# Optimization experiments

Measured on AMD Instinct MI355X. Metric: run time of the kernel, lower is better.

The kernel has to match this reference:

```python
import jax, jax.numpy as jnp
import numpy as np

# dims
B, L, D = 16, 1024, 64          # batch, seq_len==node_num, d_model==feature_dim
DI, S, R, K = 128, 16, 4, 4     # d_inner=expand*d_model, d_state, dt_rank=ceil(D/16), conv kernel
H = 256                         # ffn hidden_dimention
N, ED, CK, PL = 1024, 10, 3, 96 # node_num, embed_dim, cheb_k, pred_len
NUM_LAYERS = 2


def setup_inputs() -> dict:
    key = jax.random.key(0)
    ks = iter(jax.random.split(key, 64))
    nrm = lambda shape, s=0.02: jax.random.normal(next(ks), shape, jnp.float32) * s
    inp = {"x": jax.random.normal(next(ks), (B, L, D), jnp.float32)}
    for pre in ("fw", "bw"):
        inp[pre + "_in"] = nrm((D, 2 * DI))
        inp[pre + "_conv_w"] = nrm((DI, K), 0.1)
        inp[pre + "_conv_b"] = jnp.zeros((DI,), jnp.float32)
        inp[pre + "_xproj"] = nrm((DI, R + 2 * S))
        inp[pre + "_dtw"] = nrm((R, DI))
        inp[pre + "_dtb"] = jnp.full((DI,), -4.6, jnp.float32)  # softplus -> small dt
        inp[pre + "_Alog"] = jnp.log(jnp.tile(jnp.arange(1, S + 1, dtype=jnp.float32), (DI, 1)))
        inp[pre + "_D"] = jnp.ones((DI,), jnp.float32)
        inp[pre + "_out"] = nrm((DI, D))
    inp["ln1_g"] = jnp.ones((D,), jnp.float32); inp["ln1_b"] = jnp.zeros((D,), jnp.float32)
    inp["ffn_w1"] = nrm((D, H)); inp["ffn_b1"] = jnp.zeros((H,), jnp.float32)
    inp["ffn_w2"] = nrm((H, D)); inp["ffn_b2"] = jnp.zeros((D,), jnp.float32)
    inp["ln2_g"] = jnp.ones((D,), jnp.float32); inp["ln2_b"] = jnp.zeros((D,), jnp.float32)
    inp["node_emb"] = nrm((N, ED), 0.1)
    inp["W_pool"] = nrm((ED, CK, D, D))
    inp["b_pool"] = nrm((ED, D))
    inp["proj_w"] = nrm((D, PL)); inp["proj_b"] = jnp.zeros((PL,), jnp.float32)
    return inp


def _layernorm(x, g, b):
    m = x.mean(-1, keepdims=True)
    v = ((x - m) ** 2).mean(-1, keepdims=True)
    return (x - m) * jax.lax.rsqrt(v + 1e-5) * g + b


def _mamba_dir(x, Wi, cw, cb, Wx, Wdt, bdt, Alog, Dp, Wo):
    # x: [B,L,D] -> selective-scan SSM output [B,L,D]
    Lx = x.shape[1]
    xz = x @ Wi                                   # [B,L,2*DI]
    xc, z = jnp.split(xz, 2, axis=-1)
    xp = jnp.pad(xc, ((0, 0), (K - 1, 0), (0, 0)))  # causal depthwise conv
    xc = sum(xp[:, k:k + Lx, :] * cw[:, k] for k in range(K)) + cb
    xc = jax.nn.silu(xc)
    dbc = xc @ Wx                                 # [B,L,R+2S]
    dt = jax.nn.softplus(dbc[..., :R] @ Wdt + bdt)  # [B,L,DI]
    Bm = dbc[..., R:R + S]                        # [B,L,S]
    Cm = dbc[..., R + S:]                         # [B,L,S]
    A = -jnp.exp(Alog)                            # [DI,S]
    dA = jnp.exp(dt[..., None] * A)               # [B,L,DI,S]
    dBx = dt[..., None] * Bm[:, :, None, :] * xc[..., None]  # [B,L,DI,S]

    def step(h, ins):
        dA_t, dBx_t, C_t = ins
        h = h * dA_t + dBx_t                      # [B,DI,S]
        y = jnp.einsum('bds,bs->bd', h, C_t)
        return h, y

    h0 = jnp.zeros((x.shape[0], DI, S), x.dtype)
    _, ys = jax.lax.scan(step, h0, (jnp.moveaxis(dA, 1, 0), jnp.moveaxis(dBx, 1, 0), jnp.moveaxis(Cm, 1, 0)))
    y = jnp.moveaxis(ys, 0, 1) + Dp * xc
    y = y * jax.nn.silu(z)
    return y @ Wo


def _forward(x,
             fw_in, fw_conv_w, fw_conv_b, fw_xproj, fw_dtw, fw_dtb, fw_Alog, fw_D, fw_out,
             bw_in, bw_conv_w, bw_conv_b, bw_xproj, bw_dtw, bw_dtb, bw_Alog, bw_D, bw_out,
             ln1_g, ln1_b, ffn_w1, ffn_b1, ffn_w2, ffn_b2, ln2_g, ln2_b,
             node_emb, W_pool, b_pool, proj_w, proj_b):
    # num_layers applications of the SAME (weight-tied) bidirectional Mamba block
    for _ in range(NUM_LAYERS):
        yf = _mamba_dir(x, fw_in, fw_conv_w, fw_conv_b, fw_xproj, fw_dtw, fw_dtb, fw_Alog, fw_D, fw_out)
        yb = jnp.flip(_mamba_dir(jnp.flip(x, 1), bw_in, bw_conv_w, bw_conv_b, bw_xproj, bw_dtw, bw_dtb, bw_Alog, bw_D, bw_out), 1)
        x = _layernorm(x + yf + yb, ln1_g, ln1_b)
        x = _layernorm(x + jax.nn.relu(x @ ffn_w1 + ffn_b1) @ ffn_w2 + ffn_b2, ln2_g, ln2_b)
    # adaptive Chebyshev graph convolution (AGCRN AVWGCN)
    sup = jax.nn.softmax(jax.nn.relu(node_emb @ node_emb.T), axis=-1)   # [N,N]
    cheb = [jnp.eye(N, dtype=x.dtype), sup]
    for _ in range(CK - 2):
        cheb.append(2.0 * (sup @ cheb[-1]) - cheb[-2])
    supports = jnp.stack(cheb)                                          # [CK,N,N]
    xg = jnp.einsum('knm,bmc->bknc', supports, x)                       # [B,CK,N,C]
    W = jnp.einsum('ne,ekio->nkio', node_emb, W_pool)                   # [N,CK,C,C]
    bias = node_emb @ b_pool                                            # [N,C]
    out = jnp.einsum('bknc,nkco->bno', xg, W) + bias                    # [B,N,C]
    # dropout is identity in eval; final projection to pred_len
    return out @ proj_w + proj_b                                        # [B,N,PL]


def reference(x,
              fw_in, fw_conv_w, fw_conv_b, fw_xproj, fw_dtw, fw_dtb, fw_Alog, fw_D, fw_out,
              bw_in, bw_conv_w, bw_conv_b, bw_xproj, bw_dtw, bw_dtb, bw_Alog, bw_D, bw_out,
              ln1_g, ln1_b, ffn_w1, ffn_b1, ffn_w2, ffn_b2, ln2_g, ln2_b,
              node_emb, W_pool, b_pool, proj_w, proj_b):
    return _forward(x,
                    fw_in, fw_conv_w, fw_conv_b, fw_xproj, fw_dtw, fw_dtb, fw_Alog, fw_D, fw_out,
                    bw_in, bw_conv_w, bw_conv_b, bw_xproj, bw_dtw, bw_dtb, bw_Alog, bw_D, bw_out,
                    ln1_g, ln1_b, ffn_w1, ffn_b1, ffn_w2, ffn_b2, ln2_g, ln2_b,
                    node_emb, W_pool, b_pool, proj_w, proj_b)
```

## Files before the change

### kernel.cpp

```cpp
#include <hip/hip_runtime.h>
#include <cstddef>

#define LSEQ   1024
#define BATCH  16
#define NSTATE 16
#define BLROWS 16384
#define NNODES 1024

typedef unsigned short ushort_t;
typedef __attribute__((ext_vector_type(8))) short short8;
typedef __attribute__((ext_vector_type(4))) float f32x4;

__device__ __forceinline__ ushort_t f2bf(float f){
  union { float f; unsigned u; } v; v.f = f;
  unsigned r = v.u + 0x7fffu + ((v.u >> 16) & 1u);
  return (ushort_t)(r >> 16);
}
__device__ __forceinline__ float bf2f(ushort_t u){
  union { unsigned u; float f; } v; v.u = ((unsigned)u) << 16; return v.f;
}
__device__ __forceinline__ unsigned cvtpk(float a, float b){
  unsigned r;
  asm("v_cvt_pk_bf16_f32 %0, %1, %2" : "=v"(r) : "v"(a), "v"(b));
  return r;
}

__global__ __launch_bounds__(256) void prep_kernel(
    const float* __restrict__ x, float* __restrict__ xc, ushort_t* __restrict__ xbf,
    const float* w0, const float* w1, const float* w2, const float* w3,
    const float* w4, const float* w5, const float* w6,
    const float* w7, const float* w8, ushort_t* dst)
{
  const int bi = blockIdx.x, tid = threadIdx.x;
  if (bi < 4096){
    int i = bi * 256 + tid;
    float v = x[i];
    xc[i] = v; xbf[i] = f2bf(v);
    return;
  }
  int blk = bi - 4096;
  if (blk == 0 || blk == 1){
    const float* src = blk ? w1 : w0;
    int off = blk ? 16384 : 0;
    for (int i = tid; i < 16384; i += 256){
      int n = i / 64, k = i % 64;
      dst[off + i] = f2bf(src[k * 256 + n]);
    }
  } else if (blk == 2 || blk == 3){
    const float* src = (blk == 3) ? w3 : w2;
    int coff = (blk == 3) ? 128 : 0;
    for (int i = tid; i < 8192; i += 256){
      int o = i / 128, k = i % 128;
      dst[32768 + o * 256 + coff + k] = f2bf(src[k * 64 + o]);
    }
  } else if (blk == 4){
    for (int i = tid; i < 16384; i += 256){
      int n = i / 64, k = i % 64;
      dst[49152 + i] = f2bf(w4[k * 256 + n]);
    }
  } else if (blk == 5){
    for (int i = tid; i < 16384; i += 256){
      int n = i / 256, k = i % 256;
      dst[65536 + i] = f2bf(w5[k * 64 + n]);
    }
  } else if (blk == 6){
    for (int i = tid; i < 6144; i += 256){
      int n = i / 64, k = i % 64;
      dst[81920 + i] = f2bf(w6[k * 96 + n]);
    }
  } else {
    const float* src = (blk == 8) ? w8 : w7;
    int off = (blk == 8) ? 96256 : 88064;
    for (int i = tid; i < 8192; i += 256){
      int n = i / 128, k = i % 128;
      dst[off + i] = (n < 36) ? f2bf(src[k * 36 + n]) : (ushort_t)0;
    }
  }
}

__global__ __launch_bounds__(256, 4) void scanblock_kernel(
    const ushort_t* __restrict__ dtRbf, const ushort_t* __restrict__ xcRbf,
    const float* __restrict__ BCm, const ushort_t* __restrict__ ZBF,
    const float* __restrict__ Df, const float* __restrict__ Db,
    const float* __restrict__ HIN,
    const ushort_t* __restrict__ WoT, const ushort_t* __restrict__ W1T,
    const ushort_t* __restrict__ W2T,
    const float* __restrict__ b1, const float* __restrict__ b2,
    const float* __restrict__ ln1g, const float* __restrict__ ln1b,
    const float* __restrict__ ln2g, const float* __restrict__ ln2b,
    float* __restrict__ XCUR, ushort_t* __restrict__ XCURbf)
{
  __shared__ float    BCl[1024];
  __shared__ ushort_t Ys[16 * 264];
  __shared__ float    x1f[16 * 68];
  __shared__ ushort_t x1b[16 * 72];
  __shared__ ushort_t Hs[16 * 264];
  __shared__ float    x2f[16 * 68];
  const int tid = threadIdx.x;
  const int lane = tid & 63, w = tid >> 6;
  const int l15 = lane & 15, quad = lane >> 4;
  const int row0 = blockIdx.x * 16;
  const int b = blockIdx.x >> 6, c = blockIdx.x & 63;
  const int n = w * 16 + l15;

  ((float4*)BCl)[tid] = ((const float4*)&BCm[(size_t)row0 * 64])[tid];
  __syncthreads();

  {
    const int half = tid >> 7, d = tid & 127;
    float h[NSTATE];
    {
      size_t base = ((((size_t)half * 16 + b) * 64 + c) * 16) * 128 + d;
#pragma unroll
      for (int s = 0; s < NSTATE; s++) h[s] = HIN[base + (size_t)s * 128];
    }
    const float Dv = half ? Db[d] : Df[d];

    for (int tt = 0; tt < 16; tt++){
      int t = half ? (15 - tt) : tt;
      int row = row0 + t;
      float dtv = bf2f(dtRbf[(size_t)row * 256 + half * 128 + d]);
      float xcv = bf2f(xcRbf[(size_t)row * 256 + half * 128 + d]);
      float sgz = bf2f(ZBF[(size_t)row * 256 + half * 128 + d]);
      float c0 = dtv * xcv;
      const float4* B4 = (const float4*)&BCl[t * 64 + half * 32];
      float4 b0 = B4[0], b1v = B4[1], b2v = B4[2], b3 = B4[3];
      float Bsr[NSTATE] = {b0.x,b0.y,b0.z,b0.w, b1v.x,b1v.y,b1v.z,b1v.w,
                           b2v.x,b2v.y,b2v.z,b2v.w, b3.x,b3.y,b3.z,b3.w};
      float4 c00 = B4[4], c1 = B4[5], c2 = B4[6], c3 = B4[7];
      float Csr[NSTATE] = {c00.x,c00.y,c00.z,c00.w, c1.x,c1.y,c1.z,c1.w,
                           c2.x,c2.y,c2.z,c2.w, c3.x,c3.y,c3.z,c3.w};
      float rv = __expf(-dtv);
      float r2 = rv * rv, r4p = r2 * r2;
      float dA0 = rv, dA1 = r2, dA2 = r2 * rv, dA3 = r4p;
      float ys0 = 0.f, ys1 = 0.f, ys2 = 0.f, ys3 = 0.f;
#pragma unroll
      for (int k = 0; k < 4; k++){
        int s = k * 4;
        h[s+0] = h[s+0] * dA0 + c0 * Bsr[s+0]; ys0 += h[s+0] * Csr[s+0];
        h[s+1] = h[s+1] * dA1 + c0 * Bsr[s+1]; ys1 += h[s+1] * Csr[s+1];
        h[s+2] = h[s+2] * dA2 + c0 * Bsr[s+2]; ys2 += h[s+2] * Csr[s+2];
        h[s+3] = h[s+3] * dA3 + c0 * Bsr[s+3]; ys3 += h[s+3] * Csr[s+3];
        if (k < 3){ dA0 *= r4p; dA1 *= r4p; dA2 *= r4p; dA3 *= r4p; }
      }
      float ys = (ys0 + ys1) + (ys2 + ys3);
      Ys[t * 264 + half * 128 + d] = f2bf((ys + Dv * xcv) * sgz);
    }
  }
  __syncthreads();

  {
    f32x4 acc = (f32x4){0.f, 0.f, 0.f, 0.f};
#pragma unroll
    for (int ks = 0; ks < 8; ks++){
      short8 a = *(const short8*)&Ys[l15 * 264 + ks * 32 + quad * 8];
      short8 bb = *(const short8*)&WoT[(size_t)n * 256 + ks * 32 + quad * 8];
      acc = __builtin_amdgcn_mfma_f32_16x16x32_bf16(a, bb, acc, 0, 0, 0);
    }
#pragma unroll
    for (int r = 0; r < 4; r++){
      int lr = quad * 4 + r;
      x1f[lr * 68 + n] = acc[r] + XCUR[(size_t)(row0 + lr) * 64 + n];
    }
  }
  __syncthreads();

  {
    int r = tid >> 4, li = tid & 15;
    float4 v = *(float4*)&x1f[r * 68 + li * 4];
    float s = v.x + v.y + v.z + v.w;
    s += __shfl_xor(s, 1); s += __shfl_xor(s, 2);
    s += __shfl_xor(s, 4); s += __shfl_xor(s, 8);
    float m = s * (1.f / 64.f);
    float q = (v.x-m)*(v.x-m) + (v.y-m)*(v.y-m) + (v.z-m)*(v.z-m) + (v.w-m)*(v.w-m);
    q += __shfl_xor(q, 1); q += __shfl_xor(q, 2);
    q += __shfl_xor(q, 4); q += __shfl_xor(q, 8);
    float wsc = rsqrtf(q * (1.f / 64.f) + 1e-5f);
    float vv[4] = {v.x, v.y, v.z, v.w};
#pragma unroll
    for (int j = 0; j < 4; j++){
      int col = li * 4 + j;
      float o = (vv[j] - m) * wsc * ln1g[col] + ln1b[col];
      x1f[r * 68 + col] = o;
      x1b[r * 72 + col] = f2bf(o);
    }
  }
  __syncthreads();

  {
    f32x4 acc1[4];
#pragma unroll
    for (int f = 0; f < 4; f++) acc1[f] = (f32x4){0.f, 0.f, 0.f, 0.f};
#pragma unroll
    for (int ks = 0; ks < 2; ks++){
      short8 a = *(const short8*)&x1b[l15 * 72 + ks * 32 + quad * 8];
#pragma unroll
      for (int f = 0; f < 4; f++){
        int hc = w * 64 + f * 16 + l15;
        short8 bb = *(const short8*)&W1T[(size_t)hc * 64 + ks * 32 + quad * 8];
        acc1[f] = __builtin_amdgcn_mfma_f32_16x16x32_bf16(a, bb, acc1[f], 0, 0, 0);
      }
    }
#pragma unroll
    for (int f = 0; f < 4; f++){
      int hc = w * 64 + f * 16 + l15;
      float bv = b1[hc];
#pragma unroll
      for (int r = 0; r < 4; r++)
        Hs[(quad * 4 + r) * 264 + hc] = f2bf(fmaxf(acc1[f][r] + bv, 0.f));
    }
  }
  __syncthreads();

  {
    f32x4 acc2 = (f32x4){0.f, 0.f, 0.f, 0.f};
#pragma unroll
    for (int ks = 0; ks < 8; ks++){
      short8 a = *(const short8*)&Hs[l15 * 264 + ks * 32 + quad * 8];
      short8 bb = *(const short8*)&W2T[(size_t)n * 256 + ks * 32 + quad * 8];
      acc2 = __builtin_amdgcn_mfma_f32_16x16x32_bf16(a, bb, acc2, 0, 0, 0);
    }
    float bv = b2[n];
#pragma unroll
    for (int r = 0; r < 4; r++){
      int lr = quad * 4 + r;
      x2f[lr * 68 + n] = acc2[r] + bv + x1f[lr * 68 + n];
    }
  }
  __syncthreads();

  {
    int r = tid >> 4, li = tid & 15;
    float4 v = *(float4*)&x2f[r * 68 + li * 4];
    float s = v.x + v.y + v.z + v.w;
    s += __shfl_xor(s, 1); s += __shfl_xor(s, 2);
    s += __shfl_xor(s, 4); s += __shfl_xor(s, 8);
    float m = s * (1.f / 64.f);
    float q = (v.x-m)*(v.x-m) + (v.y-m)*(v.y-m) + (v.z-m)*(v.z-m) + (v.w-m)*(v.w-m);
    q += __shfl_xor(q, 1); q += __shfl_xor(q, 2);
    q += __shfl_xor(q, 4); q += __shfl_xor(q, 8);
    float wsc = rsqrtf(q * (1.f / 64.f) + 1e-5f);
    float vv[4] = {v.x, v.y, v.z, v.w};
#pragma unroll
    for (int j = 0; j < 4; j++){
      int col = li * 4 + j;
      float o = (vv[j] - m) * wsc * ln2g[col] + ln2b[col];
      XCUR[(size_t)(row0 + r) * 64 + col] = o;
      XCURbf[(size_t)(row0 + r) * 64 + col] = f2bf(o);
    }
  }
}

__global__ __launch_bounds__(256) void dbcdt_kernel(
    const ushort_t* __restrict__ XB,
    const ushort_t* __restrict__ WIN,
    ushort_t* __restrict__ ZBF,
    const float* cwf, const float* cbf, const ushort_t* wxtf,
    const float* wdtf, const float* bdtf,
    const float* cwb, const float* cbb, const ushort_t* wxtb,
    const float* wdtb, const float* bdtb,
    ushort_t* __restrict__ xcRbf, ushort_t* __restrict__ dtRbf,
    float* __restrict__ BCm, float* __restrict__ HLOC, float* __restrict__ PST)
{
  __shared__ ushort_t As[32 * 72];
  __shared__ ushort_t xzl[19 * 132];
  __shared__ ushort_t dtl[16 * 136];
  __shared__ float dbcs[16][40];
  const int tid = threadIdx.x;
  const int lane = tid & 63, w = tid >> 6;
  const int l15 = lane & 15, quad = lane >> 4;
  const int dir = (blockIdx.x >= 1024) ? 1 : 0;
  const int chunk = blockIdx.x & 1023;
  const int row0 = chunk * 16;
  const int t0 = row0 & (LSEQ - 1);
  const float*    cw  = dir ? cwb  : cwf;
  const float*    cb  = dir ? cbb  : cbf;
  const ushort_t* WxT = dir ? wxtb : wxtf;
  const float*    Wdt = dir ? wdtb : wdtf;
  const float*    bdt = dir ? bdtb : bdtf;

  {
    const int abase = row0 + (dir ? 0 : -3);
    int r = tid >> 3, ko = (tid & 7) * 8;
    uint4 v = {0u, 0u, 0u, 0u};
    bool zero = (r >= 19) ||
                (dir == 0 && t0 == 0 && r < 3) ||
                (dir == 1 && t0 == LSEQ - 16 && r >= 16);
    if (!zero) v = *(const uint4*)&XB[(size_t)(abase + r) * 64 + ko];
    *(uint4*)&As[r * 72 + ko] = v;
  }
  __syncthreads();

  {
    f32x4 xacc[2][4];
#pragma unroll
    for (int mt = 0; mt < 2; mt++)
#pragma unroll
      for (int f = 0; f < 4; f++) xacc[mt][f] = (f32x4){0.f, 0.f, 0.f, 0.f};
    const ushort_t* Wd = &WIN[(size_t)dir * 256 * 64];
#pragma unroll
    for (int ks = 0; ks < 2; ks++){
      short8 a0 = *(const short8*)&As[(l15) * 72 + ks * 32 + quad * 8];
      short8 a1 = *(const short8*)&As[(16 + l15) * 72 + ks * 32 + quad * 8];
#pragma unroll
      for (int f = 0; f < 4; f++){
        short8 b = *(const short8*)&Wd[(size_t)((w * 4 + f) * 16 + l15) * 64 + ks * 32 + quad * 8];
        xacc[0][f] = __builtin_amdgcn_mfma_f32_16x16x32_bf16(a0, b, xacc[0][f], 0, 0, 0);
        xacc[1][f] = __builtin_amdgcn_mfma_f32_16x16x32_bf16(a1, b, xacc[1][f], 0, 0, 0);
      }
    }
    const int zoff = dir ? 0 : 3;
#pragma unroll
    for (int mt = 0; mt < 2; mt++){
#pragma unroll
      for (int f = 0; f < 4; f++){
        int col = (w * 4 + f) * 16 + l15;
        if (col < 128){
#pragma unroll
          for (int rp = 0; rp < 2; rp++){
            unsigned pk = cvtpk(xacc[mt][f][rp*2], xacc[mt][f][rp*2+1]);
            int rowl = mt * 16 + quad * 4 + rp * 2;
            if (rowl < 19)     xzl[rowl * 132 + col]       = (ushort_t)pk;
            if (rowl + 1 < 19) xzl[(rowl + 1) * 132 + col] = (ushort_t)(pk >> 16);
          }
        } else {
          int cz = col - 128;
#pragma unroll
          for (int rp = 0; rp < 2; rp++){
            float va = xacc[mt][f][rp*2], vb = xacc[mt][f][rp*2+1];
            va = va / (1.f + __expf(-va));
            vb = vb / (1.f + __expf(-vb));
            unsigned pk = cvtpk(va, vb);
            int rowl = mt * 16 + quad * 4 + rp * 2;
            int ta = rowl - zoff, tb = rowl + 1 - zoff;
            if ((unsigned)ta < 16u)
              ZBF[(size_t)(row0 + ta) * 256 + dir * 128 + cz] = (ushort_t)pk;
            if ((unsigned)tb < 16u)
              ZBF[(size_t)(row0 + tb) * 256 + dir * 128 + cz] = (ushort_t)(pk >> 16);
          }
        }
      }
    }
  }
  __syncthreads();

  const int dd0 = tid & 127;
  const int rb = tid >> 7;
  float cr[8];
  {
    float rowv[11];
#pragma unroll
    for (int j = 0; j < 11; j++)
      rowv[j] = bf2f(xzl[(rb * 8 + j) * 132 + dd0]);
    float w0 = cw[dd0*4+0], w1 = cw[dd0*4+1], w2 = cw[dd0*4+2], w3 = cw[dd0*4+3];
    float cbv = cb[dd0];
#pragma unroll
    for (int p = 0; p < 8; p++){
      float v;
      if (dir == 0)
        v = cbv + w0*rowv[p] + w1*rowv[p+1] + w2*rowv[p+2] + w3*rowv[p+3];
      else
        v = cbv + w3*rowv[p] + w2*rowv[p+1] + w1*rowv[p+2] + w0*rowv[p+3];
      float sig = 1.f / (1.f + __expf(-v));
      cr[p] = v * sig;
    }
  }
  __syncthreads();
  ushort_t* xcl = xzl;
#pragma unroll
  for (int p = 0; p < 4; p++){
    unsigned pk = cvtpk(cr[2*p], cr[2*p+1]);
    int r = rb * 8 + 2 * p;
    xcl[r * 136 + dd0]       = (ushort_t)pk;
    xcl[(r + 1) * 136 + dd0] = (ushort_t)(pk >> 16);
    xcRbf[(size_t)(row0 + r) * 256 + dir * 128 + dd0]     = (ushort_t)pk;
    xcRbf[(size_t)(row0 + r + 1) * 256 + dir * 128 + dd0] = (ushort_t)(pk >> 16);
  }
  __syncthreads();

  {
    f32x4 pacc = (f32x4){0.f,0.f,0.f,0.f};
#pragma unroll
    for (int ks = 0; ks < 4; ks++){
      short8 a = *(const short8*)&xcl[l15 * 136 + ks * 32 + quad * 8];
      short8 b = *(const short8*)&WxT[(size_t)(w * 16 + l15) * 128 + ks * 32 + quad * 8];
      pacc = __builtin_amdgcn_mfma_f32_16x16x32_bf16(a, b, pacc, 0, 0, 0);
    }
    int col = w * 16 + l15;
    if (col < 36){
#pragma unroll
      for (int r = 0; r < 4; r++)
        dbcs[quad * 4 + r][col] = pacc[r];
    }
  }
  __syncthreads();

  {
    float w0d = Wdt[dd0], w1d = Wdt[128 + dd0], w2d = Wdt[256 + dd0],
          w3d = Wdt[384 + dd0], b0d = bdt[dd0];
    float dtvv[8];
#pragma unroll
    for (int k = 0; k < 8; k++){
      int r = rb + 2 * k;
      float u = b0d + dbcs[r][0]*w0d + dbcs[r][1]*w1d
                    + dbcs[r][2]*w2d + dbcs[r][3]*w3d;
      dtvv[k] = (u > 20.f) ? u : __logf(1.f + __expf(u));
    }
#pragma unroll
    for (int k = 0; k < 4; k++){
      unsigned pk = cvtpk(dtvv[2*k], dtvv[2*k+1]);
      int r0 = rb + 4 * k, r1 = r0 + 2;
      dtl[r0 * 136 + dd0] = (ushort_t)pk;
      dtl[r1 * 136 + dd0] = (ushort_t)(pk >> 16);
      dtRbf[(size_t)(row0 + r0) * 256 + dir * 128 + dd0] = (ushort_t)pk;
      dtRbf[(size_t)(row0 + r1) * 256 + dir * 128 + dd0] = (ushort_t)(pk >> 16);
    }
  }
  {
    int r = tid >> 4, s = tid & 15;
    BCm[(size_t)(row0 + r) * 64 + dir * 32 + s]      = dbcs[r][4 + s];
    BCm[(size_t)(row0 + r) * 64 + dir * 32 + 16 + s] = dbcs[r][20 + s];
  }
  __syncthreads();

  {
    const int shalf = tid >> 7, d = tid & 127;
    const int b = chunk >> 6, c = chunk & 63;
    float h[8];
#pragma unroll
    for (int i = 0; i < 8; i++) h[i] = 0.f;
    float sdt = 0.f;
    for (int rr2 = 0; rr2 < 16; rr2++){
      int r = dir ? (15 - rr2) : rr2;
      float dtv = bf2f(dtl[r * 136 + d]);
      sdt += dtv;
      float rv = __expf(-dtv);
      float xcv = bf2f(xcl[r * 136 + d]);
      float c0 = dtv * xcv;
      float r2 = rv * rv, r4p = r2 * r2;
      float a0;
      if (shalf){ float r8 = r4p * r4p; a0 = r8 * rv; }
      else a0 = rv;
      float a1 = a0 * rv, a2 = a0 * r2, a3 = a1 * r2;
      const float* Bp = &dbcs[r][4 + shalf * 8];
      h[0] = h[0] * a0 + c0 * Bp[0];
      h[1] = h[1] * a1 + c0 * Bp[1];
      h[2] = h[2] * a2 + c0 * Bp[2];
      h[3] = h[3] * a3 + c0 * Bp[3];
      a0 *= r4p; a1 *= r4p; a2 *= r4p; a3 *= r4p;
      h[4] = h[4] * a0 + c0 * Bp[4];
      h[5] = h[5] * a1 + c0 * Bp[5];
      h[6] = h[6] * a2 + c0 * Bp[6];
      h[7] = h[7] * a3 + c0 * Bp[7];
    }
    float e1 = __expf(-sdt);
    float base;
    if (shalf){ float e2 = e1*e1, e4 = e2*e2, e8 = e4*e4; base = e8 * e1; }
    else base = e1;
    float P[8];
    P[0] = base;
#pragma unroll
    for (int i = 1; i < 8; i++) P[i] = P[i-1] * e1;

    size_t ob = ((((size_t)dir * 16 + b) * 64 + c) * 16 + shalf * 8) * 128 + d;
#pragma unroll
    for (int i = 0; i < 8; i++){
      HLOC[ob + (size_t)i * 128] = h[i];
      PST [ob + (size_t)i * 128] = P[i];
    }
  }
}

__global__ __launch_bounds__(512) void scan_p2_kernel(
    const float* __restrict__ HLOC, float* __restrict__ PST)
{
  __shared__ float hspec[4][128];
  __shared__ float qend[4][128];
  const int tid = threadIdx.x;
  const int d = tid & 127, seg = tid >> 7;
  const int bi = blockIdx.x;
  const int s = bi & 15, b = (bi >> 4) & 15, dir = bi >> 8;
  size_t base = (((size_t)(dir * 16 + b) * 64) * 16 + s) * 128 + d;

  float spec[16], Qa[16];
  float h = 0.f, Q = 1.f;
#pragma unroll
  for (int i = 0; i < 16; i++){
    int sp = seg * 16 + i;
    int c = dir ? (63 - sp) : sp;
    size_t o = base + (size_t)c * 2048;
    float hl = HLOC[o];
    float pv = PST[o];
    spec[i] = h; Qa[i] = Q;
    h = pv * h + hl;
    Q *= pv;
  }
  hspec[seg][d] = h;
  qend[seg][d] = Q;
  __syncthreads();
  float hin = 0.f;
  for (int j = 0; j < seg; j++) hin = hspec[j][d] + qend[j][d] * hin;
#pragma unroll
  for (int i = 0; i < 16; i++){
    int sp = seg * 16 + i;
    int c = dir ? (63 - sp) : sp;
    size_t o = base + (size_t)c * 2048;
    PST[o] = spec[i] + Qa[i] * hin;
  }
}

__global__ __launch_bounds__(256) void gprep_kernel(
    const float* __restrict__ E, ushort_t* __restrict__ supbf,
    const float* __restrict__ xcur, ushort_t* __restrict__ XTTbf,
    ushort_t* __restrict__ Acat,
    const float* __restrict__ Wp, ushort_t* __restrict__ WT2)
{
  __shared__ float smemf[5760];
  const int bi = blockIdx.x, tid = threadIdx.x;

  if (bi < 1024){
    float* wmax = smemf;
    float* wsum = smemf + 8;
    int n = bi;
    float e[10];
#pragma unroll
    for (int i = 0; i < 10; i++) e[i] = E[n * 10 + i];
    float vals[4]; float mx = 0.f;
#pragma unroll
    for (int j = 0; j < 4; j++){
      int m = tid + j * 256;
      const float* Em = &E[m * 10];
      float s = 0.f;
#pragma unroll
      for (int i = 0; i < 10; i++) s += e[i] * Em[i];
      s = fmaxf(s, 0.f);
      vals[j] = s; mx = fmaxf(mx, s);
    }
    for (int off = 32; off; off >>= 1) mx = fmaxf(mx, __shfl_xor(mx, off));
    if ((tid & 63) == 0) wmax[tid >> 6] = mx;
    __syncthreads();
    mx = fmaxf(fmaxf(wmax[0], wmax[1]), fmaxf(wmax[2], wmax[3]));
    float sum = 0.f;
#pragma unroll
    for (int j = 0; j < 4; j++){ vals[j] = __expf(vals[j] - mx); sum += vals[j]; }
    for (int off = 32; off; off >>= 1) sum += __shfl_xor(sum, off);
    if ((tid & 63) == 0) wsum[tid >> 6] = sum;
    __syncthreads();
    sum = wsum[0] + wsum[1] + wsum[2] + wsum[3];
    float inv = 1.f / sum;
#pragma unroll
    for (int j = 0; j < 4; j++)
      supbf[(size_t)n * NNODES + tid + j * 256] = f2bf(vals[j] * inv);
  } else if (bi < 1280){
    float (*tile)[65] = (float(*)[65])smemf;
    const int idx = bi - 1024;
    const int b = idx >> 4, nb = idx & 15;
    const int c = tid & 63, nr = tid >> 6;
#pragma unroll
    for (int p = 0; p < 16; p++){
      int n = nr + p * 4;
      float v = xcur[(((size_t)b << 10) + nb * 64 + n) * 64 + c];
      tile[n][c] = v;
    }
    __syncthreads();
#pragma unroll
    for (int p = 0; p < 16; p++){
      int n = nr + p * 4;
      Acat[(size_t)(nb * 64 + n) * 3072 + b * 192 + c] = f2bf(tile[n][c]);
    }
#pragma unroll
    for (int p = 0; p < 16; p++){
      int cc = nr + p * 4;
      int nn = c;
      XTTbf[(size_t)(b * 64 + cc) * 1024 + nb * 64 + nn] = f2bf(tile[nn][cc]);
    }
  } else {
    float* Es = smemf;
    float* Wt = smemf + 640;
    const int idx = bi - 1280;
    const int fk = idx % 24;
    const int fn = fk / 6, ks = fk % 6;
    const int g0 = (idx / 24) * 64;
    for (int i = tid; i < 640; i += 256) Es[i] = E[g0 * 10 + i];
    for (int i = tid; i < 5120; i += 256){
      int e = i >> 9, r = i & 511;
      int kcl = r >> 4, ol = r & 15;
      Wt[e * 512 + ol * 32 + kcl] =
          Wp[(size_t)e * 12288 + (ks * 32 + kcl) * 64 + fn * 16 + ol];
    }
    __syncthreads();
    const int nl = tid >> 2, kh = tid & 3;
    const float* Ev = &Es[nl * 10];
    ushort_t outv[128];
#pragma unroll
    for (int ol = 0; ol < 16; ol++){
#pragma unroll
      for (int jj = 0; jj < 8; jj++){
        int kc = kh * 8 + jj;
        float v = 0.f;
#pragma unroll
        for (int e = 0; e < 10; e++) v += Ev[e] * Wt[e * 512 + ol * 32 + kc];
        outv[ol * 8 + jj] = f2bf(v);
      }
    }
    size_t dst = (size_t)(g0 + nl) * 12288 + fk * 512 + kh * 128;
#pragma unroll
    for (int i = 0; i < 16; i++)
      *(uint4*)&WT2[dst + i * 8] = *(uint4*)&outv[i * 8];
  }
}

template<int MODE>
__global__ __launch_bounds__(256) void mfma_g_kernel(
    const ushort_t* __restrict__ Abf, const ushort_t* __restrict__ BTbf,
    ushort_t* __restrict__ CTbf, ushort_t* __restrict__ Acat)
{
  __shared__ ushort_t As[32 * 72];
  __shared__ ushort_t Bs[32 * 72];
  const int tid = threadIdx.x;
  const int lane = tid & 63, w = tid >> 6;
  const int bm = blockIdx.y, bn = blockIdx.x;
  const int mw = (w & 1) * 16, nw = (w >> 1) * 16;
  const int l15 = lane & 15, quad = lane >> 4;

  f32x4 acc = (f32x4){0.f, 0.f, 0.f, 0.f};

  const int ar = tid >> 3, ak = (tid & 7) * 8;
  const size_t agbase = (size_t)(bm * 32 + ar) * 1024 + ak;
  const size_t bgbase = (size_t)(bn * 32 + ar) * 1024 + ak;

  for (int k0 = 0; k0 < 1024; k0 += 64){
    *(uint4*)&As[ar * 72 + ak] = *(const uint4*)&Abf[agbase + k0];
    *(uint4*)&Bs[ar * 72 + ak] = *(const uint4*)&BTbf[bgbase + k0];
    __syncthreads();
#pragma unroll
    for (int ks = 0; ks < 2; ks++){
      short8 a = *(const short8*)&As[(mw + l15) * 72 + ks * 32 + quad * 8];
      short8 b = *(const short8*)&Bs[(nw + l15) * 72 + ks * 32 + quad * 8];
      acc = __builtin_amdgcn_mfma_f32_16x16x32_bf16(a, b, acc, 0, 0, 0);
    }
    __syncthreads();
  }

  {
    int gm0 = bm * 32 + mw + quad * 4;
    int gn  = bn * 32 + nw + l15;
    int bidx = gn >> 6, cidx = gn & 63;
    if (MODE == 0){
      unsigned long long pk = 0;
#pragma unroll
      for (int r = 0; r < 4; r++){
        ushort_t h = f2bf(acc[r]);
        pk |= (unsigned long long)h << (16 * r);
        Acat[(size_t)(gm0 + r) * 3072 + bidx * 192 + 64 + cidx] = h;
      }
      *(unsigned long long*)&CTbf[(size_t)gn * 1024 + gm0] = pk;
    } else {
#pragma unroll
      for (int r = 0; r < 4; r++){
        size_t arow = (size_t)(gm0 + r) * 3072 + bidx * 192;
        float xv = bf2f(Acat[arow + cidx]);
        Acat[arow + 128 + cidx] = f2bf(2.f * acc[r] - xv);
      }
    }
  }
}

__global__ __launch_bounds__(256) void out1_kernel(
    const ushort_t* __restrict__ Acat, const ushort_t* __restrict__ WT2,
    const ushort_t* __restrict__ pwT, const float* __restrict__ E,
    const float* __restrict__ bp, const float* __restrict__ pb,
    float* __restrict__ out)
{
  __shared__ ushort_t AsL[4 * 16 * 200];
  __shared__ ushort_t PW[96 * 72];
  __shared__ ushort_t o1s[4 * 16 * 72];
  __shared__ float biasn[4][64];
  const int tid = threadIdx.x;
  const int lane = tid & 63, w = tid >> 6;
  const int l15 = lane & 15, quad = lane >> 4;
  const int n0 = blockIdx.x * 4;

  for (int p = 0; p < 6; p++){
    int f8 = tid + p * 256;
    int idx = f8 * 8;
    int nl = idx / 3072, rem = idx % 3072;
    int b = rem / 192, kc = rem % 192;
    *(uint4*)&AsL[nl * 3200 + b * 200 + kc] =
        *(const uint4*)&Acat[(size_t)(n0 + nl) * 3072 + rem];
  }
  for (int p = 0; p < 3; p++){
    int f8 = tid + p * 256;
    int idx = f8 * 8;
    int pr = idx / 64, kk = idx % 64;
    *(uint4*)&PW[pr * 72 + kk] = *(const uint4*)&pwT[idx];
  }
  {
    int nl = tid >> 6, o = tid & 63;
    float s = 0.f;
#pragma unroll
    for (int e = 0; e < 10; e++) s += E[(n0 + nl) * 10 + e] * bp[e * 64 + o];
    biasn[nl][o] = s;
  }
  __syncthreads();

  const int node = n0 + w;
  f32x4 acc[4];
#pragma unroll
  for (int f = 0; f < 4; f++) acc[f] = (f32x4){0.f, 0.f, 0.f, 0.f};
#pragma unroll
  for (int ks = 0; ks < 6; ks++){
    short8 a = *(const short8*)&AsL[w * 3200 + l15 * 200 + ks * 32 + quad * 8];
#pragma unroll
    for (int fn = 0; fn < 4; fn++){
      short8 b = *(const short8*)&WT2[(size_t)(((node * 4 + fn) * 6 + ks) * 64 + lane) * 8];
      acc[fn] = __builtin_amdgcn_mfma_f32_16x16x32_bf16(a, b, acc[fn], 0, 0, 0);
    }
  }
#pragma unroll
  for (int fn = 0; fn < 4; fn++){
    int o = fn * 16 + l15;
    float bv = biasn[w][o];
#pragma unroll
    for (int r = 0; r < 4; r++)
      o1s[w * 1152 + (quad * 4 + r) * 72 + o] = f2bf(acc[fn][r] + bv);
  }
  __syncthreads();

  f32x4 acc2[6];
#pragma unroll
  for (int f = 0; f < 6; f++) acc2[f] = (f32x4){0.f, 0.f, 0.f, 0.f};
#pragma unroll
  for (int ks = 0; ks < 2; ks++){
    short8 a = *(const short8*)&o1s[w * 1152 + l15 * 72 + ks * 32 + quad * 8];
#pragma unroll
    for (int fn = 0; fn < 6; fn++){
      short8 b = *(const short8*)&PW[(fn * 16 + l15) * 72 + ks * 32 + quad * 8];
      acc2[fn] = __builtin_amdgcn_mfma_f32_16x16x32_bf16(a, b, acc2[fn], 0, 0, 0);
    }
  }
#pragma unroll
  for (int fn = 0; fn < 6; fn++){
    int pcol = fn * 16 + l15;
    float pbv = pb[pcol];
#pragma unroll
    for (int r = 0; r < 4; r++){
      int b = quad * 4 + r;
      out[((size_t)b * 1024 + node) * 96 + pcol] = acc2[fn][r] + pbv;
    }
  }
}

extern "C" void kernel_launch(void* const* d_in, const int* in_sizes, int n_in,
                              void* d_out, int out_size, void* d_ws, size_t ws_size,
                              hipStream_t stream)
{
  const float* x_in = (const float*)d_in[0];
  const float* p_in[2]     = {(const float*)d_in[1],  (const float*)d_in[10]};
  const float* p_convw[2]  = {(const float*)d_in[2],  (const float*)d_in[11]};
  const float* p_convb[2]  = {(const float*)d_in[3],  (const float*)d_in[12]};
  const float* p_xproj[2]  = {(const float*)d_in[4],  (const float*)d_in[13]};
  const float* p_dtw[2]    = {(const float*)d_in[5],  (const float*)d_in[14]};
  const float* p_dtb[2]    = {(const float*)d_in[6],  (const float*)d_in[15]};
  const float* p_D[2]      = {(const float*)d_in[8],  (const float*)d_in[17]};
  const float* p_out[2]    = {(const float*)d_in[9],  (const float*)d_in[18]};
  const float* ln1_g = (const float*)d_in[19];
  const float* ln1_b = (const float*)d_in[20];
  const float* ffn_w1 = (const float*)d_in[21];
  const float* ffn_b1 = (const float*)d_in[22];
  const float* ffn_w2 = (const float*)d_in[23];
  const float* ffn_b2 = (const float*)d_in[24];
  const float* ln2_g = (const float*)d_in[25];
  const float* ln2_b = (const float*)d_in[26];
  const float* node_emb = (const float*)d_in[27];
  const float* W_pool   = (const float*)d_in[28];
  const float* b_pool   = (const float*)d_in[29];
  const float* proj_w   = (const float*)d_in[30];
  const float* proj_b   = (const float*)d_in[31];

  float* ws = (float*)d_ws;
  float*    HLOC   = ws;
  ushort_t* ZBF    = (ushort_t*)(ws + 4194304);
  ushort_t* XCRbf  = (ushort_t*)(ws + 6291456);
  ushort_t* DTRbf  = (ushort_t*)(ws + 10485760);
  float*    BCm    = ws + 14680064;
  float*    PST    = ws + 17825792;
  float*    XCUR   = ws + 25690112;
  ushort_t* XCURbf = (ushort_t*)(ws + 26738688);
  ushort_t* WTS    = (ushort_t*)(ws + 27262976);
  ushort_t* SUPbf  = (ushort_t*)ws;
  ushort_t* XTTbf  = (ushort_t*)(ws + 524288);
  ushort_t* XG1Tbf = (ushort_t*)(ws + 1048576);
  ushort_t* Acat   = (ushort_t*)(ws + 1572864);
  ushort_t* WT2    = (ushort_t*)(ws + 3145728);

  prep_kernel<<<4105, 256, 0, stream>>>(
      x_in, XCUR, XCURbf,
      p_in[0], p_in[1], p_out[0], p_out[1], ffn_w1, ffn_w2, proj_w,
      p_xproj[0], p_xproj[1], WTS);

  for (int layer = 0; layer < 2; layer++){
    dbcdt_kernel<<<2048, 256, 0, stream>>>(
        XCURbf, WTS, ZBF,
        p_convw[0], p_convb[0], WTS + 88064, p_dtw[0], p_dtb[0],
        p_convw[1], p_convb[1], WTS + 96256, p_dtw[1], p_dtb[1],
        XCRbf, DTRbf, BCm, HLOC, PST);
    scan_p2_kernel<<<512, 512, 0, stream>>>(HLOC, PST);
    scanblock_kernel<<<1024, 256, 0, stream>>>(
        DTRbf, XCRbf, BCm, ZBF, p_D[0], p_D[1], PST,
        WTS + 32768, WTS + 49152, WTS + 65536,
        ffn_b1, ffn_b2, ln1_g, ln1_b, ln2_g, ln2_b, XCUR, XCURbf);
  }

  gprep_kernel<<<1664, 256, 0, stream>>>(node_emb, SUPbf, XCUR, XTTbf, Acat,
                                         W_pool, WT2);
  mfma_g_kernel<0><<<dim3(32, 32), 256, 0, stream>>>(SUPbf, XTTbf, XG1Tbf, Acat);
  mfma_g_kernel<1><<<dim3(32, 32), 256, 0, stream>>>(SUPbf, XG1Tbf, nullptr, Acat);
  out1_kernel<<<256, 256, 0, stream>>>(Acat, WT2, WTS + 81920, node_emb,
                                       b_pool, proj_b, (float*)d_out);
  (void)in_sizes; (void)n_in; (void)out_size; (void)ws_size;
}
```

Measured before the change: 321.7 us.

## Store per-chunk dt sum instead of decay products; recompute decays in scan pass

The chunk kernel now writes a single summed dt per channel instead of 16 per-state decay products. The second scan pass recomputes each state's decay as exp(-(s+1)*sdt), which cuts the partial-state write and read traffic roughly in half. The input prep is also vectorised to float4 with packed bf16 conversion, and the scan-block loop prefetches the next timestep's dt, x and gate values. The cost is an extra exp per element in the scan pass and a new workspace region.

```diff
diff --git a/kernel.cpp b/kernel.cpp
--- a/kernel.cpp
+++ b/kernel.cpp
@@ -32,13 +32,17 @@
     const float* w7, const float* w8, ushort_t* dst)
 {
   const int bi = blockIdx.x, tid = threadIdx.x;
-  if (bi < 4096){
+  if (bi < 1024){
     int i = bi * 256 + tid;
-    float v = x[i];
-    xc[i] = v; xbf[i] = f2bf(v);
+    float4 v = ((const float4*)x)[i];
+    ((float4*)xc)[i] = v;
+    uint2 pk;
+    pk.x = cvtpk(v.x, v.y);
+    pk.y = cvtpk(v.z, v.w);
+    *(uint2*)&xbf[(size_t)i * 4] = pk;
     return;
   }
-  int blk = bi - 4096;
+  int blk = bi - 1024;
   if (blk == 0 || blk == 1){
     const float* src = blk ? w1 : w0;
     int off = blk ? 16384 : 0;
@@ -116,12 +120,22 @@
     }
     const float Dv = half ? Db[d] : Df[d];
 
+    int tf = half ? 15 : 0;
+    size_t idn = (size_t)(row0 + tf) * 256 + half * 128 + d;
+    float dtv_n = bf2f(dtRbf[idn]);
+    float xcv_n = bf2f(xcRbf[idn]);
+    float sgz_n = bf2f(ZBF[idn]);
+
     for (int tt = 0; tt < 16; tt++){
       int t = half ? (15 - tt) : tt;
-      int row = row0 + t;
-      float dtv = bf2f(dtRbf[(size_t)row * 256 + half * 128 + d]);
-      float xcv = bf2f(xcRbf[(size_t)row * 256 + half * 128 + d]);
-      float sgz = bf2f(ZBF[(size_t)row * 256 + half * 128 + d]);
+      float dtv = dtv_n, xcv = xcv_n, sgz = sgz_n;
+      if (tt < 15){
+        int t2 = half ? (14 - tt) : (tt + 1);
+        size_t i2 = (size_t)(row0 + t2) * 256 + half * 128 + d;
+        dtv_n = bf2f(dtRbf[i2]);
+        xcv_n = bf2f(xcRbf[i2]);
+        sgz_n = bf2f(ZBF[i2]);
+      }
       float c0 = dtv * xcv;
       const float4* B4 = (const float4*)&BCl[t * 64 + half * 32];
       float4 b0 = B4[0], b1v = B4[1], b2v = B4[2], b3 = B4[3];
@@ -260,7 +274,7 @@
     const float* cwb, const float* cbb, const ushort_t* wxtb,
     const float* wdtb, const float* bdtb,
     ushort_t* __restrict__ xcRbf, ushort_t* __restrict__ dtRbf,
-    float* __restrict__ BCm, float* __restrict__ HLOC, float* __restrict__ PST)
+    float* __restrict__ BCm, float* __restrict__ HLOC, float* __restrict__ SDT)
 {
   __shared__ ushort_t As[32 * 72];
   __shared__ ushort_t xzl[19 * 132];
@@ -453,26 +467,19 @@
       h[6] = h[6] * a2 + c0 * Bp[6];
       h[7] = h[7] * a3 + c0 * Bp[7];
     }
-    float e1 = __expf(-sdt);
-    float base;
-    if (shalf){ float e2 = e1*e1, e4 = e2*e2, e8 = e4*e4; base = e8 * e1; }
-    else base = e1;
-    float P[8];
-    P[0] = base;
-#pragma unroll
-    for (int i = 1; i < 8; i++) P[i] = P[i-1] * e1;
+    if (shalf == 0)
+      SDT[(((size_t)dir * 16 + b) * 64 + c) * 128 + d] = sdt;
 
     size_t ob = ((((size_t)dir * 16 + b) * 64 + c) * 16 + shalf * 8) * 128 + d;
 #pragma unroll
-    for (int i = 0; i < 8; i++){
+    for (int i = 0; i < 8; i++)
       HLOC[ob + (size_t)i * 128] = h[i];
-      PST [ob + (size_t)i * 128] = P[i];
-    }
   }
 }
 
 __global__ __launch_bounds__(512) void scan_p2_kernel(
-    const float* __restrict__ HLOC, float* __restrict__ PST)
+    const float* __restrict__ HLOC, const float* __restrict__ SDT,
+    float* __restrict__ PST)
 {
   __shared__ float hspec[4][128];
   __shared__ float qend[4][128];
@@ -481,6 +488,8 @@
   const int bi = blockIdx.x;
   const int s = bi & 15, b = (bi >> 4) & 15, dir = bi >> 8;
   size_t base = (((size_t)(dir * 16 + b) * 64) * 16 + s) * 128 + d;
+  size_t sbase = (((size_t)dir * 16 + b) * 64) * 128 + d;
+  const float nsp1 = -(float)(s + 1);
 
   float spec[16], Qa[16];
   float h = 0.f, Q = 1.f;
@@ -490,7 +499,7 @@
     int c = dir ? (63 - sp) : sp;
     size_t o = base + (size_t)c * 2048;
     float hl = HLOC[o];
-    float pv = PST[o];
+    float pv = __expf(nsp1 * SDT[sbase + (size_t)c * 128]);
     spec[i] = h; Qa[i] = Q;
     h = pv * h + hl;
     Q *= pv;
@@ -785,6 +794,7 @@
   ushort_t* DTRbf  = (ushort_t*)(ws + 10485760);
   float*    BCm    = ws + 14680064;
   float*    PST    = ws + 17825792;
+  float*    SDT    = ws + 22020096;
   float*    XCUR   = ws + 25690112;
   ushort_t* XCURbf = (ushort_t*)(ws + 26738688);
   ushort_t* WTS    = (ushort_t*)(ws + 27262976);
@@ -794,7 +804,7 @@
   ushort_t* Acat   = (ushort_t*)(ws + 1572864);
   ushort_t* WT2    = (ushort_t*)(ws + 3145728);
 
-  prep_kernel<<<4105, 256, 0, stream>>>(
+  prep_kernel<<<1033, 256, 0, stream>>>(
       x_in, XCUR, XCURbf,
       p_in[0], p_in[1], p_out[0], p_out[1], ffn_w1, ffn_w2, proj_w,
       p_xproj[0], p_xproj[1], WTS);
@@ -804,8 +814,8 @@
         XCURbf, WTS, ZBF,
         p_convw[0], p_convb[0], WTS + 88064, p_dtw[0], p_dtb[0],
         p_convw[1], p_convb[1], WTS + 96256, p_dtw[1], p_dtb[1],
-        XCRbf, DTRbf, BCm, HLOC, PST);
-    scan_p2_kernel<<<512, 512, 0, stream>>>(HLOC, PST);
+        XCRbf, DTRbf, BCm, HLOC, SDT);
+    scan_p2_kernel<<<512, 512, 0, stream>>>(HLOC, SDT, PST);
     scanblock_kernel<<<1024, 256, 0, stream>>>(
         DTRbf, XCRbf, BCm, ZBF, p_D[0], p_D[1], PST,
         WTS + 32768, WTS + 49152, WTS + 65536,
```

After: 380.2 us. +18.2%, slower.
